# Kernel tuning notes

Measured on AMD Instinct MI355X. Metric: run time of the kernel, lower is better.

Reference implementation:

```python
import jax, jax.numpy as jnp
import numpy as np

B, ENC, T, DIM, VOCAB = 16, 512, 64, 768, 21128
SCALE = 1.0 / np.sqrt(DIM)
NEG = -1e30
EPS = 1e-6


def setup_inputs() -> dict:
    key = jax.random.key(0)
    ks = jax.random.split(key, 20)
    def lin(k, out_f, in_f):
        k1, k2 = jax.random.split(k)
        bound = 1.0 / np.sqrt(in_f)
        W = jax.random.uniform(k1, (out_f, in_f), jnp.float32, -bound, bound)
        b = jax.random.uniform(k2, (out_f,), jnp.float32, -bound, bound)
        return W, b
    W_r, b_r = lin(ks[5], DIM, 3 * DIM)
    W_u, b_u = lin(ks[6], DIM, 3 * DIM)
    W_c, b_c = lin(ks[7], DIM, 3 * DIM)
    W_out, b_out = lin(ks[8], DIM, DIM)
    W_copy, b_copy = lin(ks[9], DIM, DIM)
    W_mode, b_mode = lin(ks[10], 1, DIM)
    return {
        "input_ids": jax.random.randint(ks[0], (B, ENC), 0, VOCAB, dtype=jnp.int32),
        "input_context": jax.random.normal(ks[1], (B, ENC, DIM), jnp.float32),
        "context_mask": jnp.ones((B, ENC), jnp.float32),
        "decode_input": jax.random.randint(ks[2], (B, T), 0, VOCAB, dtype=jnp.int32),
        "decode_target": jax.random.randint(ks[3], (B, T), 0, VOCAB, dtype=jnp.int32),
        "use_beam_search": 0,
        "beam_width": 1,
        "emb_W": jax.random.normal(ks[4], (VOCAB, DIM), jnp.float32) * 0.02,
        "W_r": W_r, "b_r": b_r,
        "W_u": W_u, "b_u": b_u,
        "W_c": W_c, "b_c": b_c,
        "W_out": W_out, "b_out": b_out,
        "W_copy": W_copy, "b_copy": b_copy,
        "W_mode": W_mode, "b_mode": b_mode,
        "init_h": jax.random.normal(ks[11], (1, DIM), jnp.float32) * 0.02,
    }


def _decode(input_ids, input_context, context_mask, decode_emb, emb_W,
            W_r, b_r, W_u, b_u, W_c, b_c, W_out, b_out, W_copy, b_copy,
            W_mode, b_mode, init_h):
    mask_add = (1.0 - context_mask) * NEG  # (B, ENC)
    rows = jnp.arange(B)[:, None]

    def step(h, emb_t):
        # attention over encoder context
        score = jnp.einsum('bsd,bd->bs', input_context, h) * SCALE + mask_add
        attn = jax.nn.softmax(score, axis=-1)
        attn_vec = jnp.einsum('bs,bsd->bd', attn, input_context)
        x = jnp.concatenate([attn_vec, emb_t, h], axis=-1)  # (B, 3*DIM)
        r = jax.nn.sigmoid(x @ W_r.T + b_r)
        u = jax.nn.sigmoid(x @ W_u.T + b_u)
        xc = jnp.concatenate([attn_vec, emb_t, r * h], axis=-1)
        c = jnp.tanh(xc @ W_c.T + b_c)
        h_new = (1.0 - u) * h + u * c
        # generate distribution (tied embedding softmax)
        out = h_new @ W_out.T + b_out
        vocab_prob = jax.nn.softmax(out @ emb_W.T, axis=-1)  # (B, VOCAB)
        # copy distribution over source positions
        copy_q = h_new @ W_copy.T + b_copy
        copy_logits = jnp.einsum('bd,bsd->bs', copy_q, input_context) + mask_add
        input_prob = jax.nn.softmax(copy_logits, axis=-1)
        mode = jax.nn.sigmoid(h_new @ W_mode.T + b_mode)  # (B, 1)
        vp = vocab_prob * mode
        vp = vp.at[rows, input_ids].add(input_prob * (1.0 - mode))
        return h_new, vp

    h0 = jnp.broadcast_to(init_h, (B, DIM))
    _, probs = jax.lax.scan(step, h0, decode_emb)  # probs: (T, B, VOCAB)
    return probs


def reference(input_ids, input_context, context_mask, decode_input, decode_target,
              use_beam_search, beam_width, emb_W, W_r, b_r, W_u, b_u, W_c, b_c,
              W_out, b_out, W_copy, b_copy, W_mode, b_mode, init_h):
    decode_emb = jnp.transpose(emb_W[decode_input], (1, 0, 2))  # (T, B, DIM)
    probs = _decode(input_ids, input_context, context_mask, decode_emb, emb_W,
                    W_r, b_r, W_u, b_u, W_c, b_c, W_out, b_out, W_copy, b_copy,
                    W_mode, b_mode, init_h)
    predict = jnp.transpose(probs, (1, 0, 2)).reshape(-1, VOCAB)  # (B*T, VOCAB)
    tgt = decode_target.reshape(-1)
    p = predict[jnp.arange(tgt.shape[0]), tgt]
    nz = (tgt != 0).astype(jnp.float32)
    loss = jnp.sum(-jnp.log(p + EPS) * nz) / jnp.sum(nz)
    return jnp.full((B,), loss)
```

## Files before the change

kernel.cpp:

```cpp
#include <hip/hip_runtime.h>
#include <hip/hip_bf16.h>
#include <math.h>

#define Bdim 16
#define ENC 512
#define Tn 64
#define DIM 768
#define VOCAB 21128
#define SCALEF 0.03608439182435161f
#define NEGF   -1e30f
#define NBLK 256
#define DYN_LDS (100 * 1024)

__device__ __forceinline__ float wred_sum(float v) {
#pragma unroll
  for (int m = 32; m >= 1; m >>= 1) v += __shfl_xor(v, m, 64);
  return v;
}
__device__ __forceinline__ float sigmf(float x) { return 1.0f / (1.0f + __expf(-x)); }

__device__ __forceinline__ void astore(float* p, float v) {
  __hip_atomic_store(p, v, __ATOMIC_RELAXED, __HIP_MEMORY_SCOPE_AGENT);
}
__device__ __forceinline__ void astore2(float* p, float a, float b) {
  float2 v = make_float2(a, b);
  __hip_atomic_store((unsigned long long*)p, *(unsigned long long*)&v,
                     __ATOMIC_RELAXED, __HIP_MEMORY_SCOPE_AGENT);
}
__device__ __forceinline__ float aloadf(const float* p) {
  return __hip_atomic_load(const_cast<float*>(p), __ATOMIC_RELAXED, __HIP_MEMORY_SCOPE_AGENT);
}
__device__ __forceinline__ unsigned afadd(unsigned* p) {
  return __hip_atomic_fetch_add(p, 1u, __ATOMIC_RELAXED, __HIP_MEMORY_SCOPE_AGENT);
}
__device__ __forceinline__ unsigned aloadu(const unsigned* p) {
  return __hip_atomic_load(const_cast<unsigned*>(p), __ATOMIC_RELAXED, __HIP_MEMORY_SCOPE_AGENT);
}

__device__ __forceinline__ void gbar(unsigned* leaf, unsigned* root, int idx, int xcd) {
  __syncthreads();
  if (threadIdx.x == 0) {
    asm volatile("s_waitcnt vmcnt(0)" ::: "memory");
    unsigned prev = afadd(&leaf[(idx * 8 + xcd) * 16]);
    if (((prev + 1u) & 31u) == 0u) afadd(&root[idx * 16]);
    while (aloadu(&root[idx * 16]) < 8u) __builtin_amdgcn_s_sleep(1);
  }
  __syncthreads();
}
__device__ __forceinline__ void lbar(unsigned* lbc, int xcd, unsigned tgt) {
  __syncthreads();
  if (threadIdx.x == 0) {
    asm volatile("s_waitcnt vmcnt(0)" ::: "memory");
    afadd(&lbc[xcd * 16]);
    while (aloadu(&lbc[xcd * 16]) < tgt) __builtin_amdgcn_s_sleep(1);
  }
  __syncthreads();
}

__device__ __forceinline__ unsigned int f2bf(float f) {
  unsigned int u = __float_as_uint(f);
  u += 0x7fffu + ((u >> 16) & 1u);
  return u >> 16;
}
__device__ __forceinline__ float bflo(unsigned int p) { return __uint_as_float(p << 16); }
__device__ __forceinline__ float bfhi(unsigned int p) { return __uint_as_float(p & 0xffff0000u); }

__global__ void k_zero_coh(unsigned long long* __restrict__ p, int n64) {
  int i = blockIdx.x * blockDim.x + threadIdx.x;
  int st = gridDim.x * blockDim.x;
  for (; i < n64; i += st)
    __hip_atomic_store(&p[i], 0ULL, __ATOMIC_RELAXED, __HIP_MEMORY_SCOPE_AGENT);
}

__global__ void k_h0(const float* __restrict__ init_h, float* __restrict__ h_all) {
  int i = blockIdx.x * blockDim.x + threadIdx.x;
  if (i < Bdim * DIM) h_all[i] = init_h[i % DIM];
}

__global__ void __launch_bounds__(256, 2) k_pre(
    const int* __restrict__ din, const float* __restrict__ emb,
    const float* __restrict__ Wr, const float* __restrict__ br,
    const float* __restrict__ Wu, const float* __restrict__ bu,
    const float* __restrict__ Wc, const float* __restrict__ bc,
    float* __restrict__ P_ru, float* __restrict__ P_c) {
  const int nb = blockIdx.x, tbc = blockIdx.y;
  const int n = nb * 256 + threadIdx.x;
  const float* wrow;
  float bias;
  if (n < 768)       { wrow = Wr + n * 2304 + 768;          bias = br[n]; }
  else if (n < 1536) { wrow = Wu + (n - 768) * 2304 + 768;  bias = bu[n - 768]; }
  else               { wrow = Wc + (n - 1536) * 2304 + 768; bias = bc[n - 1536]; }
  int id[16];
#pragma unroll
  for (int i = 0; i < 16; ++i) {
    int row = tbc * 16 + i;
    id[i] = din[(row & 15) * Tn + (row >> 4)];
  }
  float acc[16];
#pragma unroll
  for (int i = 0; i < 16; ++i) acc[i] = bias;
  for (int k = 0; k < DIM; k += 4) {
    float4 w = *(const float4*)(wrow + k);
#pragma unroll
    for (int i = 0; i < 16; ++i) {
      float4 x = *(const float4*)(emb + (size_t)id[i] * DIM + k);
      acc[i] = fmaf(w.x, x.x, fmaf(w.y, x.y, fmaf(w.z, x.z, fmaf(w.w, x.w, acc[i]))));
    }
  }
#pragma unroll
  for (int i = 0; i < 16; ++i) {
    int row = tbc * 16 + i;
    if (n < 1536) P_ru[(size_t)row * 1536 + n] = acc[i];
    else          P_c[(size_t)row * 768 + (n - 1536)] = acc[i];
  }
}

__global__ void __launch_bounds__(512, 1) k_seq(
    const float* __restrict__ ctx, const float* __restrict__ mask,
    const float* __restrict__ Wr, const float* __restrict__ Wu,
    const float* __restrict__ Wc,
    const float* __restrict__ P_ru, const float* __restrict__ P_c,
    float* __restrict__ h_all, float* __restrict__ attnc,
    float* __restrict__ r_coh, float* __restrict__ pbuf,
    float* __restrict__ psum,
    unsigned* __restrict__ slotctr, unsigned* __restrict__ leaf,
    unsigned* __restrict__ root, unsigned* __restrict__ lbc) {
  extern __shared__ float dynpad[];
  float* ctx_lds = dynpad;
  float* e_lds   = dynpad + 24576;
  float* pred    = dynpad + 24576 + 32;
  float* psh     = dynpad + 24576 + 32 + 816;
  __shared__ int slot_sh;
  const int tid = threadIdx.x;
  const int lane = tid & 63;
  const int wv = tid >> 6;
  int xcd;
  asm volatile("s_getreg_b32 %0, hwreg(HW_REG_XCC_ID)" : "=s"(xcd));
  xcd &= 7;
  if (tid == 0) slot_sh = (int)afadd(&slotctr[xcd * 16]);
  __syncthreads();
  const int slot = slot_sh;
  const int gid = xcd * 32 + slot;
  const int bA = 2 * xcd + (slot & 1);
  const int chunk = slot >> 1;
  const int dsl = chunk * 48;
  const int rg0 = gid * 3;
  const int cg0 = gid * 3;
  const int b0 = 2 * wv;

  {
    const float* chunkbase = ctx + ((size_t)(bA * ENC + chunk * 32)) * DIM;
#pragma unroll
    for (int k = 0; k < 12; ++k) {
      const int f = k * 2048 + tid * 4;
      *(float4*)(ctx_lds + f) = *(const float4*)(chunkbase + f);
    }
  }

  unsigned int wreg[9][12];
#pragma unroll
  for (int i = 0; i < 9; ++i) {
    const float* src = (i < 3) ? (Wr + (size_t)(rg0 + i) * 2304)
                     : (i < 6) ? (Wu + (size_t)(cg0 + i - 3) * 2304)
                               : (Wc + (size_t)(cg0 + i - 6) * 2304);
#pragma unroll
    for (int j = 0; j < 6; ++j) {
      int xcol = 4 * lane + 256 * j;
      int scol = (j < 3) ? xcol : (1536 + xcol - 768);
      float4 v = *(const float4*)(src + scol);
      wreg[i][2 * j]     = (f2bf(v.x)) | (f2bf(v.y) << 16);
      wreg[i][2 * j + 1] = (f2bf(v.z)) | (f2bf(v.w) << 16);
    }
  }
  float madd[4];
#pragma unroll
  for (int i = 0; i < 4; ++i)
    madd[i] = (1.0f - mask[bA * ENC + chunk * 32 + 4 * wv + i]) * NEGF;

  __syncthreads();

  int bidx = 0;
  for (int t = 0; t < Tn; ++t) {
    {
      const float* hrow = h_all + (size_t)(t * Bdim + bA) * DIM;
      float hreg[12];
#pragma unroll
      for (int j = 0; j < 12; ++j) hreg[j] = hrow[lane + 64 * j];
#pragma unroll
      for (int i = 0; i < 4; ++i) {
        const int rr = 4 * wv + i;
        const float* crow = ctx_lds + rr * 768;
        float dot = 0.f;
#pragma unroll
        for (int j = 0; j < 12; ++j) dot = fmaf(crow[lane + 64 * j], hreg[j], dot);
        dot = wred_sum(dot);
        if (lane == 0) e_lds[rr] = __expf(fmaf(dot, SCALEF, madd[i]));
      }
    }
    __syncthreads();

    if (wv == 0) {
      float ev = (lane < 32) ? e_lds[lane] : 0.f;
      float es = wred_sum(ev);
      if (lane == 0) astore(&psum[bA * 16 + chunk], es);
    }
    if (tid < 384) {
      const int d0 = 2 * tid;
      float a0 = 0.f, a1 = 0.f;
#pragma unroll 8
      for (int r = 0; r < 32; ++r) {
        const float e = e_lds[r];
        const float2 c2 = *(const float2*)(ctx_lds + r * 768 + d0);
        a0 = fmaf(e, c2.x, a0);
        a1 = fmaf(e, c2.y, a1);
      }
      astore2(&pbuf[(size_t)(bA * 16 + chunk) * 768 + d0], a0, a1);
    }
    lbar(lbc, xcd, 32u * (unsigned)(t + 1));

    {
      const int p1 = tid >> 5, o1 = tid & 31;
      float v1 = aloadf(&pbuf[(size_t)(bA * 16 + p1) * 768 + dsl + o1]);
      float v2 = 0.f;
      int p2 = 0, o2 = 0;
      if (tid < 256) {
        p2 = tid >> 4; o2 = 32 + (tid & 15);
        v2 = aloadf(&pbuf[(size_t)(bA * 16 + p2) * 768 + dsl + o2]);
      }
      if (tid < 16) psh[tid] = aloadf(&psum[bA * 16 + tid]);
      pred[o1 * 17 + p1] = v1;
      if (tid < 256) pred[o2 * 17 + p2] = v2;
      __syncthreads();
      if (tid < 48) {
        float s = 0.f, den = 0.f;
#pragma unroll
        for (int p = 0; p < 16; ++p) { s += pred[tid * 17 + p]; den += psh[p]; }
        astore(&attnc[(size_t)(t * Bdim + bA) * DIM + dsl + tid], s / den);
      }
    }
    gbar(leaf, root, bidx++, xcd);

    float4 xv[2][6];
#pragma unroll
    for (int bb = 0; bb < 2; ++bb) {
      const int b = b0 + bb;
      const float* ab = attnc + (size_t)(t * Bdim + b) * DIM;
      const float* hb = h_all + (size_t)(t * Bdim + b) * DIM;
#pragma unroll
      for (int j = 0; j < 3; ++j)
        xv[bb][j] = *(const float4*)(ab + 4 * lane + 256 * j);
#pragma unroll
      for (int j = 0; j < 3; ++j)
        xv[bb][3 + j] = *(const float4*)(hb + 4 * lane + 256 * j);
    }
    float u_reg[3];
#pragma unroll
    for (int i = 0; i < 3; ++i) {
      float d0 = 0.f, d1 = 0.f;
#pragma unroll
      for (int j = 0; j < 6; ++j) {
        const unsigned int p0 = wreg[i][2 * j], p1 = wreg[i][2 * j + 1];
        const float w0 = bflo(p0), w1 = bfhi(p0), w2 = bflo(p1), w3 = bfhi(p1);
        d0 = fmaf(w0, xv[0][j].x, fmaf(w1, xv[0][j].y, fmaf(w2, xv[0][j].z, fmaf(w3, xv[0][j].w, d0))));
        d1 = fmaf(w0, xv[1][j].x, fmaf(w1, xv[1][j].y, fmaf(w2, xv[1][j].z, fmaf(w3, xv[1][j].w, d1))));
      }
      d0 = wred_sum(d0);
      d1 = wred_sum(d1);
      if (lane < 2) {
        const int b = b0 + lane;
        const int row = rg0 + i;
        const float s = sigmf(P_ru[(size_t)(t * Bdim + b) * 1536 + row] + (lane ? d1 : d0));
        astore(&r_coh[(size_t)(t * Bdim + b) * DIM + row], s);
      }
    }
#pragma unroll
    for (int i = 0; i < 3; ++i) {
      float d0 = 0.f, d1 = 0.f;
#pragma unroll
      for (int j = 0; j < 6; ++j) {
        const unsigned int p0 = wreg[3 + i][2 * j], p1 = wreg[3 + i][2 * j + 1];
        const float w0 = bflo(p0), w1 = bfhi(p0), w2 = bflo(p1), w3 = bfhi(p1);
        d0 = fmaf(w0, xv[0][j].x, fmaf(w1, xv[0][j].y, fmaf(w2, xv[0][j].z, fmaf(w3, xv[0][j].w, d0))));
        d1 = fmaf(w0, xv[1][j].x, fmaf(w1, xv[1][j].y, fmaf(w2, xv[1][j].z, fmaf(w3, xv[1][j].w, d1))));
      }
      d0 = wred_sum(d0);
      d1 = wred_sum(d1);
      if (lane < 2) {
        const int b = b0 + lane;
        u_reg[i] = sigmf(P_ru[(size_t)(t * Bdim + b) * 1536 + 768 + cg0 + i] + (lane ? d1 : d0));
      }
    }
    gbar(leaf, root, bidx++, xcd);

#pragma unroll
    for (int bb = 0; bb < 2; ++bb) {
      const int b = b0 + bb;
      const float* rb = r_coh + (size_t)(t * Bdim + b) * DIM;
#pragma unroll
      for (int j = 0; j < 3; ++j) {
        float4 rv = *(const float4*)(rb + 4 * lane + 256 * j);
        xv[bb][3 + j].x *= rv.x; xv[bb][3 + j].y *= rv.y;
        xv[bb][3 + j].z *= rv.z; xv[bb][3 + j].w *= rv.w;
      }
    }
#pragma unroll
    for (int i = 0; i < 3; ++i) {
      float d0 = 0.f, d1 = 0.f;
#pragma unroll
      for (int j = 0; j < 6; ++j) {
        const unsigned int p0 = wreg[6 + i][2 * j], p1 = wreg[6 + i][2 * j + 1];
        const float w0 = bflo(p0), w1 = bfhi(p0), w2 = bflo(p1), w3 = bfhi(p1);
        d0 = fmaf(w0, xv[0][j].x, fmaf(w1, xv[0][j].y, fmaf(w2, xv[0][j].z, fmaf(w3, xv[0][j].w, d0))));
        d1 = fmaf(w0, xv[1][j].x, fmaf(w1, xv[1][j].y, fmaf(w2, xv[1][j].z, fmaf(w3, xv[1][j].w, d1))));
      }
      d0 = wred_sum(d0);
      d1 = wred_sum(d1);
      if (lane < 2) {
        const int b = b0 + lane;
        const int row = cg0 + i;
        const float c = tanhf(P_c[(size_t)(t * Bdim + b) * DIM + row] + (lane ? d1 : d0));
        const float hp = h_all[(size_t)(t * Bdim + b) * DIM + row];
        astore(&h_all[(size_t)((t + 1) * Bdim + b) * DIM + row], hp + u_reg[i] * (c - hp));
      }
    }
    gbar(leaf, root, bidx++, xcd);
  }
}

__global__ void __launch_bounds__(256, 2) k_out(
    const float* __restrict__ Wo, const float* __restrict__ bo,
    const float* __restrict__ Wcp, const float* __restrict__ bcp,
    const float* __restrict__ h_all, float* __restrict__ out_all,
    float* __restrict__ copyq) {
  const int nb = blockIdx.x, tbc = blockIdx.y;
  const int n = nb * 256 + threadIdx.x;
  const float* wrow;
  float bias;
  if (n < 768) { wrow = Wo + (size_t)n * 768;          bias = bo[n]; }
  else         { wrow = Wcp + (size_t)(n - 768) * 768; bias = bcp[n - 768]; }
  const float* hbase = h_all + (size_t)(tbc * 16 + 16) * DIM;
  float acc[16];
#pragma unroll
  for (int i = 0; i < 16; ++i) acc[i] = bias;
  for (int k = 0; k < DIM; k += 4) {
    float4 w = *(const float4*)(wrow + k);
#pragma unroll
    for (int i = 0; i < 16; ++i) {
      float4 x = *(const float4*)(hbase + i * DIM + k);
      acc[i] = fmaf(w.x, x.x, fmaf(w.y, x.y, fmaf(w.z, x.z, fmaf(w.w, x.w, acc[i]))));
    }
  }
#pragma unroll
  for (int i = 0; i < 16; ++i) {
    int row = tbc * 16 + i;
    if (n < 768) out_all[(size_t)row * 768 + n] = acc[i];
    else         copyq[(size_t)row * 768 + (n - 768)] = acc[i];
  }
}

__global__ void __launch_bounds__(512, 2) k_copy(
    const int* __restrict__ ids, const int* __restrict__ dtg,
    const float* __restrict__ ctx, const float* __restrict__ mask,
    const float* __restrict__ copyq,
    float* __restrict__ cnum, float* __restrict__ cden) {
  const int sc = blockIdx.x, b = blockIdx.y;
  const int lane = threadIdx.x & 63;
  const int seg = __builtin_amdgcn_readfirstlane(threadIdx.x >> 6);
  const int s = sc * 64 + lane;
  __shared__ float part[8][64];
  float creg[96];
  const float* crow = ctx + ((size_t)(b * ENC + s)) * DIM + seg * 96;
#pragma unroll
  for (int kk = 0; kk < 96; kk += 4) {
    float4 v = *(const float4*)(crow + kk);
    creg[kk] = v.x; creg[kk + 1] = v.y; creg[kk + 2] = v.z; creg[kk + 3] = v.w;
  }
  const float madd = (1.0f - mask[b * ENC + s]) * NEGF;
  const int myid = ids[b * ENC + s];
  for (int t = 0; t < Tn; ++t) {
    const int row = t * Bdim + b;
    const float* q = copyq + (size_t)row * 768 + seg * 96;
    float dot = 0.f;
#pragma unroll
    for (int kk = 0; kk < 96; kk += 4) {
      float4 qv = *(const float4*)(q + kk);
      dot = fmaf(qv.x, creg[kk], fmaf(qv.y, creg[kk + 1],
            fmaf(qv.z, creg[kk + 2], fmaf(qv.w, creg[kk + 3], dot))));
    }
    part[seg][lane] = dot;
    __syncthreads();
    if (threadIdx.x < 64) {
      float logit = madd;
#pragma unroll
      for (int w = 0; w < 8; ++w) logit += part[w][lane];
      float e = __expf(logit);
      int tgt = dtg[b * Tn + t];
      float ne = (myid == tgt) ? e : 0.f;
      float dsum = wred_sum(e);
      float nsum = wred_sum(ne);
      if (lane == 0) {
        atomicAdd(&cden[row], dsum);
        if (nsum != 0.f) atomicAdd(&cnum[row], nsum);
      }
    }
    __syncthreads();
  }
}

__global__ void __launch_bounds__(256, 1) k_vocab(
    const float* __restrict__ emb, const float* __restrict__ out_all,
    float* __restrict__ S) {
  const int vc = blockIdx.x, tbc = blockIdx.y;
  const int tb0 = tbc * 32;
  const int v = vc * 256 + threadIdx.x;
  const bool valid = v < VOCAB;
  const int vv = valid ? v : 0;
  float acc[32];
#pragma unroll
  for (int i = 0; i < 32; ++i) acc[i] = 0.f;
  const float* erow = emb + (size_t)vv * DIM;
  for (int k = 0; k < DIM; k += 4) {
    float4 w = *(const float4*)(erow + k);
#pragma unroll
    for (int i = 0; i < 32; ++i) {
      float4 a = *(const float4*)(out_all + (size_t)(tb0 + i) * DIM + k);
      acc[i] = fmaf(w.x, a.x, fmaf(w.y, a.y, fmaf(w.z, a.z, fmaf(w.w, a.w, acc[i]))));
    }
  }
  __shared__ float rowsum[32];
  if (threadIdx.x < 32) rowsum[threadIdx.x] = 0.f;
  __syncthreads();
  const int lane = threadIdx.x & 63;
#pragma unroll
  for (int i = 0; i < 32; ++i) {
    float e = valid ? __expf(acc[i]) : 0.f;
    float r = wred_sum(e);
    if (lane == 0) atomicAdd(&rowsum[i], r);
  }
  __syncthreads();
  if (threadIdx.x < 32) atomicAdd(&S[tb0 + threadIdx.x], rowsum[threadIdx.x]);
}

__global__ void k_tgt(
    const int* __restrict__ dtg, const float* __restrict__ out_all,
    const float* __restrict__ emb, const float* __restrict__ Wm,
    const float* __restrict__ bm, const float* __restrict__ h_all,
    const float* __restrict__ S, const float* __restrict__ cnum,
    const float* __restrict__ cden, float* __restrict__ loss) {
  const int lane = threadIdx.x & 63;
  const int w = __builtin_amdgcn_readfirstlane(threadIdx.x >> 6);
  for (int rr = 0; rr < 16; ++rr) {
    const int row = (blockIdx.x * 4 + w) * 16 + rr;
    const int t = row >> 4, b = row & 15;
    const int tgt = dtg[b * Tn + t];
    const float* orow = out_all + (size_t)row * DIM + lane * 12;
    const float* erow = emb + (size_t)tgt * DIM + lane * 12;
    const float* hrow = h_all + (size_t)(row + 16) * DIM + lane * 12;
    const float* wm = Wm + lane * 12;
    float lt = 0.f, md = 0.f;
#pragma unroll
    for (int k = 0; k < 12; k += 4) {
      float4 o = *(const float4*)(orow + k);
      float4 e = *(const float4*)(erow + k);
      float4 h = *(const float4*)(hrow + k);
      float4 m = *(const float4*)(wm + k);
      lt = fmaf(o.x, e.x, fmaf(o.y, e.y, fmaf(o.z, e.z, fmaf(o.w, e.w, lt))));
      md = fmaf(m.x, h.x, fmaf(m.y, h.y, fmaf(m.z, h.z, fmaf(m.w, h.w, md))));
    }
    lt = wred_sum(lt);
    md = wred_sum(md);
    if (lane == 0 && tgt != 0) {
      float mode = sigmf(md + bm[0]);
      float pv = __expf(lt) / S[row] * mode;
      float den = cden[row];
      float pc = (den > 0.f) ? (cnum[row] / den) : 0.f;
      float p = pv + (1.0f - mode) * pc;
      atomicAdd(&loss[0], -logf(p + 1e-6f));
      atomicAdd(&loss[1], 1.0f);
    }
  }
}

__global__ void k_write(const float* __restrict__ loss, float* __restrict__ out) {
  if (threadIdx.x < Bdim) out[threadIdx.x] = loss[0] / loss[1];
}

extern "C" void kernel_launch(void* const* d_in, const int* in_sizes, int n_in,
                              void* d_out, int out_size, void* d_ws, size_t ws_size,
                              hipStream_t stream) {
  (void)in_sizes; (void)n_in; (void)out_size; (void)ws_size;
  const int*   input_ids = (const int*)d_in[0];
  const float* ctx       = (const float*)d_in[1];
  const float* cmask     = (const float*)d_in[2];
  const int*   din       = (const int*)d_in[3];
  const int*   dtg       = (const int*)d_in[4];
  const float* embW      = (const float*)d_in[7];
  const float* Wr = (const float*)d_in[8];  const float* br  = (const float*)d_in[9];
  const float* Wu = (const float*)d_in[10]; const float* bu  = (const float*)d_in[11];
  const float* Wc = (const float*)d_in[12]; const float* bc  = (const float*)d_in[13];
  const float* Wo = (const float*)d_in[14]; const float* bo  = (const float*)d_in[15];
  const float* Wcp= (const float*)d_in[16]; const float* bcp = (const float*)d_in[17];
  const float* Wm = (const float*)d_in[18]; const float* bm  = (const float*)d_in[19];
  const float* ih = (const float*)d_in[20];

  float* ws      = (float*)d_ws;
  float* P_ru    = ws;
  float* P_c     = P_ru + 1024 * 1536;
  float* h_all   = P_c + 1024 * 768;
  float* out_all = h_all + 65 * 16 * 768;
  float* copyq   = out_all + 1024 * 768;
  float* attnc   = copyq + 1024 * 768;
  float* r_coh   = attnc + 64 * 16 * 768;
  float* pbuf    = r_coh + 64 * 16 * 768;
  float* psum    = pbuf + 16 * 16 * 768;
  float* S       = psum + 256;
  float* cnum    = S + 1024;
  float* cden    = cnum + 1024;
  float* loss    = cden + 1024;
  unsigned* slotctr = (unsigned*)(loss + 32);
  unsigned* leaf    = slotctr + 8 * 16;
  unsigned* root    = leaf + 192 * 8 * 16;
  unsigned* lbc     = root + 192 * 16;
  const int nzero64 = (3 * 1024 + 32 + 8 * 16 + 192 * 8 * 16 + 192 * 16 + 8 * 16) / 2;

  hipFuncSetAttribute((const void*)k_seq,
                      hipFuncAttributeMaxDynamicSharedMemorySize, DYN_LDS);

  k_zero_coh<<<64, 1024, 0, stream>>>((unsigned long long*)S, nzero64);
  k_h0<<<12, 1024, 0, stream>>>(ih, h_all);
  k_pre<<<dim3(9, 64), 256, 0, stream>>>(din, embW, Wr, br, Wu, bu, Wc, bc, P_ru, P_c);

  k_seq<<<NBLK, 512, DYN_LDS, stream>>>(ctx, cmask, Wr, Wu, Wc, P_ru, P_c,
                                        h_all, attnc, r_coh, pbuf, psum,
                                        slotctr, leaf, root, lbc);

  k_out<<<dim3(6, 64), 256, 0, stream>>>(Wo, bo, Wcp, bcp, h_all, out_all, copyq);
  k_copy<<<dim3(8, 16), 512, 0, stream>>>(input_ids, dtg, ctx, cmask, copyq, cnum, cden);
  k_vocab<<<dim3(83, 32), 256, 0, stream>>>(embW, out_all, S);
  k_tgt<<<16, 256, 0, stream>>>(dtg, out_all, embW, Wm, bm, h_all, S, cnum, cden, loss);
  k_write<<<1, 64, 0, stream>>>(loss, (float*)d_out);
}
```

Before: 4.286 ms.

## Replace counter barriers with epoch flag barriers and widen vocab row tile

The grid and XCD-local barriers in the persistent recurrent kernel now use per-block epoch flags. Each block writes its own flag, and one wavefront polls all 32 slot flags with a wave-wide any, replacing atomic fetch-add counters on leaf and root arrays. The aim is to cut atomic contention and per-barrier latency across the 64 timesteps with their four barriers each. Separately, the vocab logsumexp kernel processes 64 rows per block instead of 32, halving reloads of the embedding matrix at the cost of 64 accumulator registers per thread.

```diff
diff --git a/kernel.cpp b/kernel.cpp
--- a/kernel.cpp
+++ b/kernel.cpp
@@ -22,6 +22,9 @@
 __device__ __forceinline__ void astore(float* p, float v) {
   __hip_atomic_store(p, v, __ATOMIC_RELAXED, __HIP_MEMORY_SCOPE_AGENT);
 }
+__device__ __forceinline__ void astoreu(unsigned* p, unsigned v) {
+  __hip_atomic_store(p, v, __ATOMIC_RELAXED, __HIP_MEMORY_SCOPE_AGENT);
+}
 __device__ __forceinline__ void astore2(float* p, float a, float b) {
   float2 v = make_float2(a, b);
   __hip_atomic_store((unsigned long long*)p, *(unsigned long long*)&v,
@@ -37,22 +40,42 @@
   return __hip_atomic_load(const_cast<unsigned*>(p), __ATOMIC_RELAXED, __HIP_MEMORY_SCOPE_AGENT);
 }
 
-__device__ __forceinline__ void gbar(unsigned* leaf, unsigned* root, int idx, int xcd) {
-  __syncthreads();
-  if (threadIdx.x == 0) {
-    asm volatile("s_waitcnt vmcnt(0)" ::: "memory");
-    unsigned prev = afadd(&leaf[(idx * 8 + xcd) * 16]);
-    if (((prev + 1u) & 31u) == 0u) afadd(&root[idx * 16]);
-    while (aloadu(&root[idx * 16]) < 8u) __builtin_amdgcn_s_sleep(1);
-  }
-  __syncthreads();
-}
-__device__ __forceinline__ void lbar(unsigned* lbc, int xcd, unsigned tgt) {
-  __syncthreads();
-  if (threadIdx.x == 0) {
-    asm volatile("s_waitcnt vmcnt(0)" ::: "memory");
-    afadd(&lbc[xcd * 16]);
-    while (aloadu(&lbc[xcd * 16]) < tgt) __builtin_amdgcn_s_sleep(1);
+__device__ __forceinline__ void lbarf(unsigned* fl, int xcd, int slot, unsigned ep) {
+  __syncthreads();
+  if (threadIdx.x < 64) {
+    if (threadIdx.x == 0) {
+      asm volatile("s_waitcnt vmcnt(0)" ::: "memory");
+      astoreu(&fl[xcd * 32 + slot], ep);
+    }
+    for (;;) {
+      unsigned v = (threadIdx.x < 32) ? aloadu(&fl[xcd * 32 + threadIdx.x]) : ep;
+      if (!__any(v < ep)) break;
+      __builtin_amdgcn_s_sleep(1);
+    }
+  }
+  __syncthreads();
+}
+__device__ __forceinline__ void gbarf(unsigned* fl, unsigned* rf, int xcd, int slot,
+                                      unsigned ep) {
+  __syncthreads();
+  if (threadIdx.x < 64) {
+    if (threadIdx.x == 0) {
+      asm volatile("s_waitcnt vmcnt(0)" ::: "memory");
+      astoreu(&fl[xcd * 32 + slot], ep);
+    }
+    if (slot == 0) {
+      for (;;) {
+        unsigned v = (threadIdx.x < 32) ? aloadu(&fl[xcd * 32 + threadIdx.x]) : ep;
+        if (!__any(v < ep)) break;
+        __builtin_amdgcn_s_sleep(1);
+      }
+      if (threadIdx.x == 0) astoreu(&rf[xcd], ep);
+    }
+    for (;;) {
+      unsigned r = (threadIdx.x < 8) ? aloadu(&rf[threadIdx.x]) : ep;
+      if (!__any(r < ep)) break;
+      __builtin_amdgcn_s_sleep(1);
+    }
   }
   __syncthreads();
 }
@@ -123,8 +146,8 @@
     float* __restrict__ h_all, float* __restrict__ attnc,
     float* __restrict__ r_coh, float* __restrict__ pbuf,
     float* __restrict__ psum,
-    unsigned* __restrict__ slotctr, unsigned* __restrict__ leaf,
-    unsigned* __restrict__ root, unsigned* __restrict__ lbc) {
+    unsigned* __restrict__ slotctr, unsigned* __restrict__ fl,
+    unsigned* __restrict__ rf) {
   extern __shared__ float dynpad[];
   float* ctx_lds = dynpad;
   float* e_lds   = dynpad + 24576;
@@ -179,7 +202,7 @@
 
   __syncthreads();
 
-  int bidx = 0;
+  unsigned ep = 1;
   for (int t = 0; t < Tn; ++t) {
     {
       const float* hrow = h_all + (size_t)(t * Bdim + bA) * DIM;
@@ -216,7 +239,7 @@
       }
       astore2(&pbuf[(size_t)(bA * 16 + chunk) * 768 + d0], a0, a1);
     }
-    lbar(lbc, xcd, 32u * (unsigned)(t + 1));
+    lbarf(fl, xcd, slot, ep++);
 
     {
       const int p1 = tid >> 5, o1 = tid & 31;
@@ -238,7 +261,7 @@
         astore(&attnc[(size_t)(t * Bdim + bA) * DIM + dsl + tid], s / den);
       }
     }
-    gbar(leaf, root, bidx++, xcd);
+    gbarf(fl, rf, xcd, slot, ep++);
 
     float4 xv[2][6];
 #pragma unroll
@@ -290,7 +313,7 @@
         u_reg[i] = sigmf(P_ru[(size_t)(t * Bdim + b) * 1536 + 768 + cg0 + i] + (lane ? d1 : d0));
       }
     }
-    gbar(leaf, root, bidx++, xcd);
+    gbarf(fl, rf, xcd, slot, ep++);
 
 #pragma unroll
     for (int bb = 0; bb < 2; ++bb) {
@@ -323,7 +346,7 @@
         astore(&h_all[(size_t)((t + 1) * Bdim + b) * DIM + row], hp + u_reg[i] * (c - hp));
       }
     }
-    gbar(leaf, root, bidx++, xcd);
+    gbarf(fl, rf, xcd, slot, ep++);
   }
 }
 
@@ -411,34 +434,35 @@
     const float* __restrict__ emb, const float* __restrict__ out_all,
     float* __restrict__ S) {
   const int vc = blockIdx.x, tbc = blockIdx.y;
-  const int tb0 = tbc * 32;
+  const int tb0 = tbc * 64;
   const int v = vc * 256 + threadIdx.x;
   const bool valid = v < VOCAB;
   const int vv = valid ? v : 0;
-  float acc[32];
-#pragma unroll
-  for (int i = 0; i < 32; ++i) acc[i] = 0.f;
+  float acc[64];
+#pragma unroll
+  for (int i = 0; i < 64; ++i) acc[i] = 0.f;
   const float* erow = emb + (size_t)vv * DIM;
+  const float* ob = out_all + (size_t)tb0 * DIM;
   for (int k = 0; k < DIM; k += 4) {
     float4 w = *(const float4*)(erow + k);
 #pragma unroll
-    for (int i = 0; i < 32; ++i) {
-      float4 a = *(const float4*)(out_all + (size_t)(tb0 + i) * DIM + k);
+    for (int i = 0; i < 64; ++i) {
+      float4 a = *(const float4*)(ob + (size_t)i * DIM + k);
       acc[i] = fmaf(w.x, a.x, fmaf(w.y, a.y, fmaf(w.z, a.z, fmaf(w.w, a.w, acc[i]))));
     }
   }
-  __shared__ float rowsum[32];
-  if (threadIdx.x < 32) rowsum[threadIdx.x] = 0.f;
+  __shared__ float rowsum[64];
+  if (threadIdx.x < 64) rowsum[threadIdx.x] = 0.f;
   __syncthreads();
   const int lane = threadIdx.x & 63;
 #pragma unroll
-  for (int i = 0; i < 32; ++i) {
+  for (int i = 0; i < 64; ++i) {
     float e = valid ? __expf(acc[i]) : 0.f;
     float r = wred_sum(e);
     if (lane == 0) atomicAdd(&rowsum[i], r);
   }
   __syncthreads();
-  if (threadIdx.x < 32) atomicAdd(&S[tb0 + threadIdx.x], rowsum[threadIdx.x]);
+  if (threadIdx.x < 64) atomicAdd(&S[tb0 + threadIdx.x], rowsum[threadIdx.x]);
 }
 
 __global__ void k_tgt(
@@ -518,10 +542,9 @@
   float* cden    = cnum + 1024;
   float* loss    = cden + 1024;
   unsigned* slotctr = (unsigned*)(loss + 32);
-  unsigned* leaf    = slotctr + 8 * 16;
-  unsigned* root    = leaf + 192 * 8 * 16;
-  unsigned* lbc     = root + 192 * 16;
-  const int nzero64 = (3 * 1024 + 32 + 8 * 16 + 192 * 8 * 16 + 192 * 16 + 8 * 16) / 2;
+  unsigned* fl      = slotctr + 128;
+  unsigned* rf      = fl + 8 * 32;
+  const int nzero64 = (3 * 1024 + 32 + 128 + 8 * 32 + 32) / 2;
 
   hipFuncSetAttribute((const void*)k_seq,
                       hipFuncAttributeMaxDynamicSharedMemorySize, DYN_LDS);
@@ -532,11 +555,11 @@
 
   k_seq<<<NBLK, 512, DYN_LDS, stream>>>(ctx, cmask, Wr, Wu, Wc, P_ru, P_c,
                                         h_all, attnc, r_coh, pbuf, psum,
-                                        slotctr, leaf, root, lbc);
+                                        slotctr, fl, rf);
 
   k_out<<<dim3(6, 64), 256, 0, stream>>>(Wo, bo, Wcp, bcp, h_all, out_all, copyq);
   k_copy<<<dim3(8, 16), 512, 0, stream>>>(input_ids, dtg, ctx, cmask, copyq, cnum, cden);
-  k_vocab<<<dim3(83, 32), 256, 0, stream>>>(embW, out_all, S);
+  k_vocab<<<dim3(83, 16), 256, 0, stream>>>(embW, out_all, S);
   k_tgt<<<16, 256, 0, stream>>>(dtg, out_all, embW, Wm, bm, h_all, S, cnum, cden, loss);
   k_write<<<1, 64, 0, stream>>>(loss, (float*)d_out);
 }
```

New measurement: 4.405 ms. +2.8%, slower.
